# Optimization experiments

Measured on AMD Instinct MI355X. Metric: run time of the kernel, lower is better.

The kernel has to match this reference:

```python
import jax, jax.numpy as jnp
import numpy as np

# --- configuration matching setup_inputs ---
N_EVENTS = 4          # number of events in the ragged batch (row_splits has 5 entries)
HITS_PER_EVENT = 50000
K_CLUSTERS = 256      # max truth shower index per event
Q_MIN = 1.0
REPULSION_CONTRIB = 0.5
SCALE = 1.0
EPS = 1e-6


def setup_inputs() -> dict:
    key = jax.random.key(0)
    k1, k2 = jax.random.split(key)
    n = N_EVENTS * HITS_PER_EVENT
    coords = jax.random.normal(k1, (n, 3), dtype=jnp.float32)
    truth_indices = jax.random.randint(k2, (n, 1), 0, K_CLUSTERS, dtype=jnp.int32)
    row_splits = (jnp.arange(N_EVENTS + 1, dtype=jnp.int32) * HITS_PER_EVENT)
    return {"coords": coords, "truth_indices": truth_indices, "row_splits": row_splits}


def _oc_cluster_loss(coords, truth_indices):
    """Object-condensation attractive/repulsive potentials.

    coords:        [n, C] float clustering coordinates (n = E * Nev, equal splits)
    truth_indices: [n, 1] int cluster id per hit, in [0, K)
    Returns (V_att, V_rep) scalars, averaged over events.
    """
    C = coords.shape[1]
    x = coords.reshape(N_EVENTS, HITS_PER_EVENT, C)            # [E, N, C]
    t = truth_indices.reshape(N_EVENTS, HITS_PER_EVENT)        # [E, N]

    # beta_like = 0.5 (3-input path of LLClusterCoordinates) -> constant charge
    beta = jnp.float32(0.5)
    q_val = jnp.arctanh(beta) ** 2 + jnp.float32(Q_MIN)        # scalar
    q = jnp.full((N_EVENTS, HITS_PER_EVENT), q_val, dtype=coords.dtype)  # [E, N]

    # membership mask (one-hot over truth clusters)
    M = jax.nn.one_hot(t, K_CLUSTERS, dtype=coords.dtype)      # [E, N, K]
    qM = M * q[..., None]                                      # [E, N, K]

    # q-weighted average condensation point per cluster (use_average_cc_pos=True)
    sum_q = jnp.sum(qM, axis=1)                                # [E, K]
    x_cc = jnp.einsum('enk,enc->ekc', qM, x) / (sum_q[..., None] + EPS)  # [E, K, C]

    # charge of the condensation (max-beta) vertex per cluster
    q_alpha = jnp.max(qM, axis=1)                              # [E, K] (0 for empty clusters)

    # pairwise hit <-> condensation-point distances
    diff = x[:, :, None, :] - x_cc[:, None, :, :]              # [E, N, K, C]
    d2 = jnp.sum(diff * diff, axis=-1)                         # [E, N, K]
    d = jnp.sqrt(d2 + EPS)

    w = q[..., None] * q_alpha[:, None, :]                     # [E, N, K]
    n_per_ev = jnp.float32(HITS_PER_EVENT)

    V_att_ev = jnp.sum(M * w * d2, axis=(1, 2)) / n_per_ev                   # [E]
    V_rep_ev = jnp.sum((1.0 - M) * w * jax.nn.relu(1.0 - d), axis=(1, 2)) / n_per_ev
    return jnp.mean(V_att_ev), jnp.mean(V_rep_ev)


def reference(coords, truth_indices, row_splits):
    V_att, V_rep = _oc_cluster_loss(coords, truth_indices)
    lossval = SCALE * ((1.0 - REPULSION_CONTRIB) * V_att + REPULSION_CONTRIB * V_rep)
    # layer returns (inputs[0], lossval) when return_lossval=True
    return coords, lossval
```

## Files before the change

### kernel.cpp

```cpp
#include <hip/hip_runtime.h>

typedef unsigned long long ull;

#define E_EVENTS 4
#define NPE 50000
#define K_CL 256
#define QV 1.30173724f
#define QV2 (QV * QV)
#define EPSF 1e-6f
#define SB 64
#define BPE 196
#define LOSS_SCALE 2.5e-6f
#define LOSS_IDX (3 * E_EVENTS * NPE)

__global__ __launch_bounds__(256) void k_sums(const float* __restrict__ coords,
                                              const int* __restrict__ truth,
                                              float* __restrict__ partial,
                                              int* __restrict__ maxn) {
    __shared__ float s[4 * K_CL];
    int tid = threadIdx.x;
    #pragma unroll
    for (int i = 0; i < 4; ++i) s[tid + 256 * i] = 0.0f;
    __syncthreads();

    int e = blockIdx.x >> 6, blk = blockIdx.x & (SB - 1);
    if (blk == 0 && tid == 0) maxn[e] = 0;
    for (int local = blk * 256 + tid; local < NPE; local += SB * 256) {
        int h = e * NPE + local;
        int t = truth[h];
        atomicAdd(&s[t],            coords[3 * h]);
        atomicAdd(&s[K_CL + t],     coords[3 * h + 1]);
        atomicAdd(&s[2 * K_CL + t], coords[3 * h + 2]);
        atomicAdd(&s[3 * K_CL + t], 1.0f);
    }
    __syncthreads();

    float* g = partial + blockIdx.x * 1024;
    #pragma unroll
    for (int i = 0; i < 4; ++i) g[tid + 256 * i] = s[tid + 256 * i];
}

__global__ __launch_bounds__(1024) void k_cc(const float* __restrict__ partial,
                                             float4* __restrict__ cc,
                                             int* __restrict__ maxn,
                                             float* __restrict__ out) {
    __shared__ float4 red[16][64];
    int tid = threadIdx.x;
    int kl = tid & 63, chunk = tid >> 6;
    int e = blockIdx.x >> 2, kg = blockIdx.x & 3;
    int k = kg * 64 + kl;

    const float* base = partial + (e * SB + chunk * 4) * 1024 + k;
    float sx = 0.f, sy = 0.f, sz = 0.f, cn = 0.f;
    #pragma unroll
    for (int j = 0; j < 4; ++j) {
        const float* p = base + j * 1024;
        sx += p[0]; sy += p[256]; sz += p[512]; cn += p[768];
    }
    red[chunk][kl] = make_float4(sx, sy, sz, cn);
    __syncthreads();
    #pragma unroll
    for (int s = 8; s > 0; s >>= 1) {
        if (chunk < s) {
            float4 a = red[chunk][kl], o = red[chunk + s][kl];
            red[chunk][kl] = make_float4(a.x + o.x, a.y + o.y,
                                         a.z + o.z, a.w + o.w);
        }
        __syncthreads();
    }

    if (chunk == 0) {
        float4 t = red[0][kl];
        float inv = QV / (QV * t.w + EPSF);
        float cx = t.x * inv, cy = t.y * inv, cz = t.z * inv;
        float ccn = fmaf(cx, cx, fmaf(cy, cy, cz * cz));
        bool empty = (t.w == 0.0f);
        cc[e * K_CL + k] = empty ? make_float4(0.f, 0.f, 0.f, 1e9f)
                                 : make_float4(cx, cy, cz, ccn);
        float nrm = empty ? 0.f : __builtin_amdgcn_sqrtf(ccn);
        #pragma unroll
        for (int o = 32; o > 0; o >>= 1)
            nrm = fmaxf(nrm, __shfl_down(nrm, o, 64));
        if (kl == 0) atomicMax(&maxn[e], __float_as_int(nrm));
        if (blockIdx.x == 0 && tid == 0) out[LOSS_IDX] = 0.0f;
    }
}

__global__ __launch_bounds__(256) void k_fused(const float* __restrict__ coords,
                                               const int* __restrict__ truth,
                                               const float4* __restrict__ cc,
                                               const int* __restrict__ maxn,
                                               float* __restrict__ out) {
    __shared__ float4 hl[256];
    __shared__ float4 scc[K_CL];
    __shared__ int bcnt;
    __shared__ float wsum[4];
    int tid = threadIdx.x;
    int lane = tid & 63, wv = tid >> 6;
    int e = blockIdx.x / BPE;
    int local = (blockIdx.x - e * BPE) * 256 + tid;
    bool valid = local < NPE;

    scc[tid] = cc[e * K_CL + tid];
    if (tid == 0) bcnt = 0;
    float M = __int_as_float(maxn[e]);
    float th = 1.0f + M + 1e-3f;
    float th2 = th * th;
    __syncthreads();

    float att = 0.0f, pp = 1e30f, x = 0.f, y = 0.f, z = 0.f;
    if (valid) {
        int h = e * NPE + local;
        x = coords[3 * h]; y = coords[3 * h + 1]; z = coords[3 * h + 2];
        int t = truth[h];
        out[3 * h] = x; out[3 * h + 1] = y; out[3 * h + 2] = z;
        float4 c = scc[t];
        float dx = x - c.x, dy = y - c.y, dz = z - c.z;
        float d2o = fmaf(dx, dx, fmaf(dy, dy, dz * dz));
        float dno = __builtin_amdgcn_sqrtf(d2o + EPSF);
        att = QV2 * (d2o - fmaxf(0.0f, 1.0f - dno));
        pp = fmaf(x, x, fmaf(y, y, z * z));
    }

    bool inner = valid && (pp < th2);
    ull mask = __ballot(inner);
    int cnt = __popcll(mask);
    if (cnt > 0) {
        int leader = __ffsll(mask) - 1;
        int base = 0;
        if (lane == leader) base = atomicAdd(&bcnt, cnt);
        base = __shfl(base, leader, 64);
        if (inner) {
            int prefix = __popcll(mask & ((1ull << lane) - 1ull));
            hl[base + prefix] = make_float4(-2.0f * x, -2.0f * y, -2.0f * z,
                                            pp + EPSF);
        }
    }
    __syncthreads();

    float4 c0 = scc[lane], c1 = scc[lane + 64];
    float4 c2 = scc[lane + 128], c3 = scc[lane + 192];
    int n = bcnt;
    float rep = 0.0f;
    #pragma unroll 2
    for (int j = wv; j < n; j += 4) {
        float4 p = hl[j];
        float a0 = fmaf(p.x, c0.x, fmaf(p.y, c0.y, fmaf(p.z, c0.z, c0.w))) + p.w;
        float a1 = fmaf(p.x, c1.x, fmaf(p.y, c1.y, fmaf(p.z, c1.z, c1.w))) + p.w;
        float a2 = fmaf(p.x, c2.x, fmaf(p.y, c2.y, fmaf(p.z, c2.z, c2.w))) + p.w;
        float a3 = fmaf(p.x, c3.x, fmaf(p.y, c3.y, fmaf(p.z, c3.z, c3.w))) + p.w;
        rep += fmaxf(0.0f, 1.0f - __builtin_amdgcn_sqrtf(a0))
             + fmaxf(0.0f, 1.0f - __builtin_amdgcn_sqrtf(a1))
             + fmaxf(0.0f, 1.0f - __builtin_amdgcn_sqrtf(a2))
             + fmaxf(0.0f, 1.0f - __builtin_amdgcn_sqrtf(a3));
    }
    float contrib = att + QV2 * rep;

    #pragma unroll
    for (int o = 32; o > 0; o >>= 1) contrib += __shfl_down(contrib, o, 64);
    if (lane == 0) wsum[wv] = contrib;
    __syncthreads();
    if (tid == 0)
        atomicAdd(out + LOSS_IDX,
                  (wsum[0] + wsum[1] + wsum[2] + wsum[3]) * LOSS_SCALE);
}

extern "C" void kernel_launch(void* const* d_in, const int* in_sizes, int n_in,
                              void* d_out, int out_size, void* d_ws, size_t ws_size,
                              hipStream_t stream) {
    const float* coords = (const float*)d_in[0];
    const int*   truth  = (const int*)d_in[1];

    char* ws = (char*)d_ws;
    float*  partial = (float*)ws;
    float4* cc      = (float4*)(ws + (1 << 20));
    int*    maxn    = (int*)(ws + (1 << 20) + 16384);
    float*  out     = (float*)d_out;

    k_sums <<<E_EVENTS * SB, 256, 0, stream>>>(coords, truth, partial, maxn);
    k_cc   <<<16, 1024, 0, stream>>>(partial, cc, maxn, out);
    k_fused<<<E_EVENTS * BPE, 256, 0, stream>>>(coords, truth, cc, maxn, out);
}
```

Before: 83.21 us.

## Fuse sum, centroid and loss kernels into one cooperative kernel with grid syncs

Merges the three launches (per-cluster sums, centroid reduction, fused loss) into a single cooperative kernel separated by two grid-wide syncs. Coordinates and truth labels are loaded once and kept in registers across phases, so the second global read disappears. Each block now builds its own shared-memory histogram, which enlarges the partials buffer; the centroid step reduces these across 64 blocks. The cost is the grid barriers plus the requirement that all 784 blocks be co-resident.

```diff
diff --git a/kernel.cpp b/kernel.cpp
--- a/kernel.cpp
+++ b/kernel.cpp
@@ -1,4 +1,7 @@
 #include <hip/hip_runtime.h>
+#include <hip/hip_cooperative_groups.h>
+
+namespace cg = cooperative_groups;
 
 typedef unsigned long long ull;
 
@@ -8,99 +11,105 @@
 #define QV 1.30173724f
 #define QV2 (QV * QV)
 #define EPSF 1e-6f
-#define SB 64
 #define BPE 196
+#define NBLK (E_EVENTS * BPE)
+#define CCBLK 64
 #define LOSS_SCALE 2.5e-6f
 #define LOSS_IDX (3 * E_EVENTS * NPE)
 
-__global__ __launch_bounds__(256) void k_sums(const float* __restrict__ coords,
-                                              const int* __restrict__ truth,
-                                              float* __restrict__ partial,
-                                              int* __restrict__ maxn) {
-    __shared__ float s[4 * K_CL];
+__global__ __launch_bounds__(256, 4) void k_all(const float* __restrict__ coords,
+                                                const int* __restrict__ truth,
+                                                float* __restrict__ partial,
+                                                float4* __restrict__ cc,
+                                                int* __restrict__ maxn,
+                                                float* __restrict__ out) {
+    __shared__ float4 shA[256];
+    __shared__ float4 shB[256];
+    __shared__ int bcnt;
+    __shared__ float wsum[4];
+
+    cg::grid_group grid = cg::this_grid();
     int tid = threadIdx.x;
+    int lane = tid & 63, wv = tid >> 6;
+    int b = blockIdx.x;
+    int e = b / BPE, lb = b - e * BPE;
+    int local = lb * 256 + tid;
+    bool valid = local < NPE;
+
+    float* hist = (float*)shA;
     #pragma unroll
-    for (int i = 0; i < 4; ++i) s[tid + 256 * i] = 0.0f;
-    __syncthreads();
-
-    int e = blockIdx.x >> 6, blk = blockIdx.x & (SB - 1);
-    if (blk == 0 && tid == 0) maxn[e] = 0;
-    for (int local = blk * 256 + tid; local < NPE; local += SB * 256) {
-        int h = e * NPE + local;
-        int t = truth[h];
-        atomicAdd(&s[t],            coords[3 * h]);
-        atomicAdd(&s[K_CL + t],     coords[3 * h + 1]);
-        atomicAdd(&s[2 * K_CL + t], coords[3 * h + 2]);
-        atomicAdd(&s[3 * K_CL + t], 1.0f);
+    for (int i = 0; i < 4; ++i) hist[tid + 256 * i] = 0.0f;
+    if (tid == 0) {
+        if (lb == 0) maxn[e] = 0;
+        if (b == 0) out[LOSS_IDX] = 0.0f;
     }
     __syncthreads();
 
-    float* g = partial + blockIdx.x * 1024;
-    #pragma unroll
-    for (int i = 0; i < 4; ++i) g[tid + 256 * i] = s[tid + 256 * i];
-}
-
-__global__ __launch_bounds__(1024) void k_cc(const float* __restrict__ partial,
-                                             float4* __restrict__ cc,
-                                             int* __restrict__ maxn,
-                                             float* __restrict__ out) {
-    __shared__ float4 red[16][64];
-    int tid = threadIdx.x;
-    int kl = tid & 63, chunk = tid >> 6;
-    int e = blockIdx.x >> 2, kg = blockIdx.x & 3;
-    int k = kg * 64 + kl;
-
-    const float* base = partial + (e * SB + chunk * 4) * 1024 + k;
-    float sx = 0.f, sy = 0.f, sz = 0.f, cn = 0.f;
-    #pragma unroll
-    for (int j = 0; j < 4; ++j) {
-        const float* p = base + j * 1024;
-        sx += p[0]; sy += p[256]; sz += p[512]; cn += p[768];
+    float x = 0.f, y = 0.f, z = 0.f, pp = 1e30f;
+    int t = 0;
+    if (valid) {
+        int h = e * NPE + local;
+        x = coords[3 * h]; y = coords[3 * h + 1]; z = coords[3 * h + 2];
+        t = truth[h];
+        out[3 * h] = x; out[3 * h + 1] = y; out[3 * h + 2] = z;
+        pp = fmaf(x, x, fmaf(y, y, z * z));
+        atomicAdd(&hist[t],            x);
+        atomicAdd(&hist[K_CL + t],     y);
+        atomicAdd(&hist[2 * K_CL + t], z);
+        atomicAdd(&hist[3 * K_CL + t], 1.0f);
     }
-    red[chunk][kl] = make_float4(sx, sy, sz, cn);
     __syncthreads();
-    #pragma unroll
-    for (int s = 8; s > 0; s >>= 1) {
-        if (chunk < s) {
-            float4 a = red[chunk][kl], o = red[chunk + s][kl];
-            red[chunk][kl] = make_float4(a.x + o.x, a.y + o.y,
-                                         a.z + o.z, a.w + o.w);
-        }
-        __syncthreads();
+    {
+        float* g = partial + b * 1024;
+        #pragma unroll
+        for (int i = 0; i < 4; ++i) g[tid + 256 * i] = hist[tid + 256 * i];
     }
 
-    if (chunk == 0) {
-        float4 t = red[0][kl];
-        float inv = QV / (QV * t.w + EPSF);
-        float cx = t.x * inv, cy = t.y * inv, cz = t.z * inv;
-        float ccn = fmaf(cx, cx, fmaf(cy, cy, cz * cz));
-        bool empty = (t.w == 0.0f);
-        cc[e * K_CL + k] = empty ? make_float4(0.f, 0.f, 0.f, 1e9f)
-                                 : make_float4(cx, cy, cz, ccn);
-        float nrm = empty ? 0.f : __builtin_amdgcn_sqrtf(ccn);
+    grid.sync();
+
+    if (b < CCBLK) {
+        int e1 = b >> 4;
+        int kg = b & 15;
+        int kl = tid & 15, cgp = tid >> 4;
+        int k = kg * 16 + kl;
+        float sx = 0.f, sy = 0.f, sz = 0.f, cn = 0.f;
+        const float* base = partial + (e1 * BPE) * 1024 + k;
+        for (int c = cgp; c < BPE; c += 16) {
+            const float* p = base + c * 1024;
+            sx += p[0]; sy += p[256]; sz += p[512]; cn += p[768];
+        }
+        float4* red = shB;
+        red[cgp * 16 + kl] = make_float4(sx, sy, sz, cn);
+        __syncthreads();
         #pragma unroll
-        for (int o = 32; o > 0; o >>= 1)
-            nrm = fmaxf(nrm, __shfl_down(nrm, o, 64));
-        if (kl == 0) atomicMax(&maxn[e], __float_as_int(nrm));
-        if (blockIdx.x == 0 && tid == 0) out[LOSS_IDX] = 0.0f;
+        for (int s = 8; s > 0; s >>= 1) {
+            if (cgp < s) {
+                float4 a = red[cgp * 16 + kl], o = red[(cgp + s) * 16 + kl];
+                red[cgp * 16 + kl] = make_float4(a.x + o.x, a.y + o.y,
+                                                 a.z + o.z, a.w + o.w);
+            }
+            __syncthreads();
+        }
+        if (cgp == 0) {
+            float4 s4 = red[kl];
+            float inv = QV / (QV * s4.w + EPSF);
+            float cx = s4.x * inv, cy = s4.y * inv, cz = s4.z * inv;
+            float ccn = fmaf(cx, cx, fmaf(cy, cy, cz * cz));
+            bool empty = (s4.w == 0.0f);
+            cc[e1 * K_CL + k] = empty ? make_float4(0.f, 0.f, 0.f, 1e9f)
+                                      : make_float4(cx, cy, cz, ccn);
+            float nrm = empty ? 0.f : __builtin_amdgcn_sqrtf(ccn);
+            #pragma unroll
+            for (int o = 8; o > 0; o >>= 1)
+                nrm = fmaxf(nrm, __shfl_down(nrm, o, 16));
+            if (kl == 0) atomicMax(&maxn[e1], __float_as_int(nrm));
+        }
     }
-}
 
-__global__ __launch_bounds__(256) void k_fused(const float* __restrict__ coords,
-                                               const int* __restrict__ truth,
-                                               const float4* __restrict__ cc,
-                                               const int* __restrict__ maxn,
-                                               float* __restrict__ out) {
-    __shared__ float4 hl[256];
-    __shared__ float4 scc[K_CL];
-    __shared__ int bcnt;
-    __shared__ float wsum[4];
-    int tid = threadIdx.x;
-    int lane = tid & 63, wv = tid >> 6;
-    int e = blockIdx.x / BPE;
-    int local = (blockIdx.x - e * BPE) * 256 + tid;
-    bool valid = local < NPE;
+    grid.sync();
 
+    float4* scc = shA;
+    float4* hl  = shB;
     scc[tid] = cc[e * K_CL + tid];
     if (tid == 0) bcnt = 0;
     float M = __int_as_float(maxn[e]);
@@ -108,18 +117,13 @@
     float th2 = th * th;
     __syncthreads();
 
-    float att = 0.0f, pp = 1e30f, x = 0.f, y = 0.f, z = 0.f;
+    float att = 0.0f;
     if (valid) {
-        int h = e * NPE + local;
-        x = coords[3 * h]; y = coords[3 * h + 1]; z = coords[3 * h + 2];
-        int t = truth[h];
-        out[3 * h] = x; out[3 * h + 1] = y; out[3 * h + 2] = z;
         float4 c = scc[t];
         float dx = x - c.x, dy = y - c.y, dz = z - c.z;
         float d2o = fmaf(dx, dx, fmaf(dy, dy, dz * dz));
         float dno = __builtin_amdgcn_sqrtf(d2o + EPSF);
         att = QV2 * (d2o - fmaxf(0.0f, 1.0f - dno));
-        pp = fmaf(x, x, fmaf(y, y, z * z));
     }
 
     bool inner = valid && (pp < th2);
@@ -127,13 +131,13 @@
     int cnt = __popcll(mask);
     if (cnt > 0) {
         int leader = __ffsll(mask) - 1;
-        int base = 0;
-        if (lane == leader) base = atomicAdd(&bcnt, cnt);
-        base = __shfl(base, leader, 64);
+        int base0 = 0;
+        if (lane == leader) base0 = atomicAdd(&bcnt, cnt);
+        base0 = __shfl(base0, leader, 64);
         if (inner) {
             int prefix = __popcll(mask & ((1ull << lane) - 1ull));
-            hl[base + prefix] = make_float4(-2.0f * x, -2.0f * y, -2.0f * z,
-                                            pp + EPSF);
+            hl[base0 + prefix] = make_float4(-2.0f * x, -2.0f * y, -2.0f * z,
+                                             pp + EPSF);
         }
     }
     __syncthreads();
@@ -173,11 +177,12 @@
 
     char* ws = (char*)d_ws;
     float*  partial = (float*)ws;
-    float4* cc      = (float4*)(ws + (1 << 20));
-    int*    maxn    = (int*)(ws + (1 << 20) + 16384);
+    float4* cc      = (float4*)(ws + (4 << 20));
+    int*    maxn    = (int*)(ws + (4 << 20) + 16384);
     float*  out     = (float*)d_out;
 
-    k_sums <<<E_EVENTS * SB, 256, 0, stream>>>(coords, truth, partial, maxn);
-    k_cc   <<<16, 1024, 0, stream>>>(partial, cc, maxn, out);
-    k_fused<<<E_EVENTS * BPE, 256, 0, stream>>>(coords, truth, cc, maxn, out);
+    void* args[6] = {(void*)&coords, (void*)&truth, (void*)&partial,
+                     (void*)&cc, (void*)&maxn, (void*)&out};
+    hipLaunchCooperativeKernel((const void*)k_all, dim3(NBLK), dim3(256),
+                               args, 0, stream);
 }
```

Result: slower. 219.1 us (+163.4%).

## Fold centroid reduction into fused kernel and vectorize per-cluster sums

Applied to the files above, without the earlier changes.

Removes the separate centroid kernel. Each fused block now reduces the per-event partial sums itself, computes the condensation points and the max norm in shared memory, and so drops one launch and the global maxn atomics. The sums kernel uses float4/int4 vector loads with 1024-thread blocks and fewer blocks per event. The fused kernel moves to 512-thread blocks, which gives larger candidate lists. The cost is that every fused block redundantly reduces 16 partial records, and the sums kernel has less parallelism.

```diff
diff --git a/kernel.cpp b/kernel.cpp
--- a/kernel.cpp
+++ b/kernel.cpp
@@ -8,105 +8,89 @@
 #define QV 1.30173724f
 #define QV2 (QV * QV)
 #define EPSF 1e-6f
-#define SB 64
-#define BPE 196
+#define SB 16
+#define FB 512
+#define BPE 98
 #define LOSS_SCALE 2.5e-6f
 #define LOSS_IDX (3 * E_EVENTS * NPE)
 
-__global__ __launch_bounds__(256) void k_sums(const float* __restrict__ coords,
-                                              const int* __restrict__ truth,
-                                              float* __restrict__ partial,
-                                              int* __restrict__ maxn) {
+__global__ __launch_bounds__(1024) void k_sums(const float4* __restrict__ c4,
+                                               const int4* __restrict__ t4,
+                                               float4* __restrict__ partial,
+                                               float* __restrict__ out) {
     __shared__ float s[4 * K_CL];
     int tid = threadIdx.x;
-    #pragma unroll
-    for (int i = 0; i < 4; ++i) s[tid + 256 * i] = 0.0f;
+    s[tid] = 0.0f;
+    if (blockIdx.x == 0 && tid == 0) out[LOSS_IDX] = 0.0f;
     __syncthreads();
 
-    int e = blockIdx.x >> 6, blk = blockIdx.x & (SB - 1);
-    if (blk == 0 && tid == 0) maxn[e] = 0;
-    for (int local = blk * 256 + tid; local < NPE; local += SB * 256) {
-        int h = e * NPE + local;
-        int t = truth[h];
-        atomicAdd(&s[t],            coords[3 * h]);
-        atomicAdd(&s[K_CL + t],     coords[3 * h + 1]);
-        atomicAdd(&s[2 * K_CL + t], coords[3 * h + 2]);
-        atomicAdd(&s[3 * K_CL + t], 1.0f);
+    int e = blockIdx.x >> 4, blk = blockIdx.x & (SB - 1);
+    const float4* cb = c4 + e * (NPE * 3 / 4);
+    const int4*   tb = t4 + e * (NPE / 4);
+    for (int g = blk * 1024 + tid; g < NPE / 4; g += SB * 1024) {
+        float4 a = cb[3 * g], b = cb[3 * g + 1], c = cb[3 * g + 2];
+        int4 t = tb[g];
+        atomicAdd(&s[t.x], a.x); atomicAdd(&s[K_CL + t.x], a.y);
+        atomicAdd(&s[2 * K_CL + t.x], a.z); atomicAdd(&s[3 * K_CL + t.x], 1.0f);
+        atomicAdd(&s[t.y], a.w); atomicAdd(&s[K_CL + t.y], b.x);
+        atomicAdd(&s[2 * K_CL + t.y], b.y); atomicAdd(&s[3 * K_CL + t.y], 1.0f);
+        atomicAdd(&s[t.z], b.z); atomicAdd(&s[K_CL + t.z], b.w);
+        atomicAdd(&s[2 * K_CL + t.z], c.x); atomicAdd(&s[3 * K_CL + t.z], 1.0f);
+        atomicAdd(&s[t.w], c.y); atomicAdd(&s[K_CL + t.w], c.z);
+        atomicAdd(&s[2 * K_CL + t.w], c.w); atomicAdd(&s[3 * K_CL + t.w], 1.0f);
     }
     __syncthreads();
-
-    float* g = partial + blockIdx.x * 1024;
-    #pragma unroll
-    for (int i = 0; i < 4; ++i) g[tid + 256 * i] = s[tid + 256 * i];
+    if (tid < K_CL)
+        partial[blockIdx.x * K_CL + tid] =
+            make_float4(s[tid], s[K_CL + tid], s[2 * K_CL + tid], s[3 * K_CL + tid]);
 }
 
-__global__ __launch_bounds__(1024) void k_cc(const float* __restrict__ partial,
-                                             float4* __restrict__ cc,
-                                             int* __restrict__ maxn,
-                                             float* __restrict__ out) {
-    __shared__ float4 red[16][64];
+__global__ __launch_bounds__(512) void k_fused(const float* __restrict__ coords,
+                                               const int* __restrict__ truth,
+                                               const float4* __restrict__ partial,
+                                               float* __restrict__ out) {
+    __shared__ float4 scc[K_CL];
+    __shared__ float4 hl[FB];
+    __shared__ int bcnt;
+    __shared__ float wsum[8], wmax[4];
     int tid = threadIdx.x;
-    int kl = tid & 63, chunk = tid >> 6;
-    int e = blockIdx.x >> 2, kg = blockIdx.x & 3;
-    int k = kg * 64 + kl;
+    int lane = tid & 63, wv = tid >> 6;
+    int e = blockIdx.x / BPE;
+    int local = (blockIdx.x - e * BPE) * FB + tid;
+    bool valid = local < NPE;
+    if (tid == 0) bcnt = 0;
 
-    const float* base = partial + (e * SB + chunk * 4) * 1024 + k;
-    float sx = 0.f, sy = 0.f, sz = 0.f, cn = 0.f;
-    #pragma unroll
-    for (int j = 0; j < 4; ++j) {
-        const float* p = base + j * 1024;
-        sx += p[0]; sy += p[256]; sz += p[512]; cn += p[768];
+    {
+        int k = tid & 255, half = tid >> 8;
+        const float4* base = partial + e * SB * K_CL + half * 8 * K_CL + k;
+        float4 acc = make_float4(0.f, 0.f, 0.f, 0.f);
+        #pragma unroll
+        for (int c = 0; c < 8; ++c) {
+            float4 p = base[c * K_CL];
+            acc.x += p.x; acc.y += p.y; acc.z += p.z; acc.w += p.w;
+        }
+        hl[tid] = acc;
     }
-    red[chunk][kl] = make_float4(sx, sy, sz, cn);
     __syncthreads();
-    #pragma unroll
-    for (int s = 8; s > 0; s >>= 1) {
-        if (chunk < s) {
-            float4 a = red[chunk][kl], o = red[chunk + s][kl];
-            red[chunk][kl] = make_float4(a.x + o.x, a.y + o.y,
-                                         a.z + o.z, a.w + o.w);
-        }
-        __syncthreads();
-    }
-
-    if (chunk == 0) {
-        float4 t = red[0][kl];
-        float inv = QV / (QV * t.w + EPSF);
-        float cx = t.x * inv, cy = t.y * inv, cz = t.z * inv;
+    if (tid < K_CL) {
+        float4 a = hl[tid], b = hl[tid + 256];
+        float sx = a.x + b.x, sy = a.y + b.y, sz = a.z + b.z, cn = a.w + b.w;
+        float inv = QV / (QV * cn + EPSF);
+        float cx = sx * inv, cy = sy * inv, cz = sz * inv;
         float ccn = fmaf(cx, cx, fmaf(cy, cy, cz * cz));
-        bool empty = (t.w == 0.0f);
-        cc[e * K_CL + k] = empty ? make_float4(0.f, 0.f, 0.f, 1e9f)
-                                 : make_float4(cx, cy, cz, ccn);
+        bool empty = (cn == 0.0f);
+        scc[tid] = empty ? make_float4(0.f, 0.f, 0.f, 1e9f)
+                         : make_float4(cx, cy, cz, ccn);
         float nrm = empty ? 0.f : __builtin_amdgcn_sqrtf(ccn);
         #pragma unroll
         for (int o = 32; o > 0; o >>= 1)
             nrm = fmaxf(nrm, __shfl_down(nrm, o, 64));
-        if (kl == 0) atomicMax(&maxn[e], __float_as_int(nrm));
-        if (blockIdx.x == 0 && tid == 0) out[LOSS_IDX] = 0.0f;
+        if (lane == 0) wmax[wv] = nrm;
     }
-}
-
-__global__ __launch_bounds__(256) void k_fused(const float* __restrict__ coords,
-                                               const int* __restrict__ truth,
-                                               const float4* __restrict__ cc,
-                                               const int* __restrict__ maxn,
-                                               float* __restrict__ out) {
-    __shared__ float4 hl[256];
-    __shared__ float4 scc[K_CL];
-    __shared__ int bcnt;
-    __shared__ float wsum[4];
-    int tid = threadIdx.x;
-    int lane = tid & 63, wv = tid >> 6;
-    int e = blockIdx.x / BPE;
-    int local = (blockIdx.x - e * BPE) * 256 + tid;
-    bool valid = local < NPE;
-
-    scc[tid] = cc[e * K_CL + tid];
-    if (tid == 0) bcnt = 0;
-    float M = __int_as_float(maxn[e]);
+    __syncthreads();
+    float M = fmaxf(fmaxf(wmax[0], wmax[1]), fmaxf(wmax[2], wmax[3]));
     float th = 1.0f + M + 1e-3f;
     float th2 = th * th;
-    __syncthreads();
 
     float att = 0.0f, pp = 1e30f, x = 0.f, y = 0.f, z = 0.f;
     if (valid) {
@@ -127,13 +111,13 @@
     int cnt = __popcll(mask);
     if (cnt > 0) {
         int leader = __ffsll(mask) - 1;
-        int base = 0;
-        if (lane == leader) base = atomicAdd(&bcnt, cnt);
-        base = __shfl(base, leader, 64);
+        int b0 = 0;
+        if (lane == leader) b0 = atomicAdd(&bcnt, cnt);
+        b0 = __shfl(b0, leader, 64);
         if (inner) {
             int prefix = __popcll(mask & ((1ull << lane) - 1ull));
-            hl[base + prefix] = make_float4(-2.0f * x, -2.0f * y, -2.0f * z,
-                                            pp + EPSF);
+            hl[b0 + prefix] = make_float4(-2.0f * x, -2.0f * y, -2.0f * z,
+                                          pp + EPSF);
         }
     }
     __syncthreads();
@@ -143,7 +127,7 @@
     int n = bcnt;
     float rep = 0.0f;
     #pragma unroll 2
-    for (int j = wv; j < n; j += 4) {
+    for (int j = wv; j < n; j += 8) {
         float4 p = hl[j];
         float a0 = fmaf(p.x, c0.x, fmaf(p.y, c0.y, fmaf(p.z, c0.z, c0.w))) + p.w;
         float a1 = fmaf(p.x, c1.x, fmaf(p.y, c1.y, fmaf(p.z, c1.z, c1.w))) + p.w;
@@ -160,9 +144,11 @@
     for (int o = 32; o > 0; o >>= 1) contrib += __shfl_down(contrib, o, 64);
     if (lane == 0) wsum[wv] = contrib;
     __syncthreads();
-    if (tid == 0)
-        atomicAdd(out + LOSS_IDX,
-                  (wsum[0] + wsum[1] + wsum[2] + wsum[3]) * LOSS_SCALE);
+    if (tid == 0) {
+        float ssum = wsum[0] + wsum[1] + wsum[2] + wsum[3]
+                   + wsum[4] + wsum[5] + wsum[6] + wsum[7];
+        atomicAdd(out + LOSS_IDX, ssum * LOSS_SCALE);
+    }
 }
 
 extern "C" void kernel_launch(void* const* d_in, const int* in_sizes, int n_in,
@@ -171,13 +157,10 @@
     const float* coords = (const float*)d_in[0];
     const int*   truth  = (const int*)d_in[1];
 
-    char* ws = (char*)d_ws;
-    float*  partial = (float*)ws;
-    float4* cc      = (float4*)(ws + (1 << 20));
-    int*    maxn    = (int*)(ws + (1 << 20) + 16384);
+    float4* partial = (float4*)d_ws;
     float*  out     = (float*)d_out;
 
-    k_sums <<<E_EVENTS * SB, 256, 0, stream>>>(coords, truth, partial, maxn);
-    k_cc   <<<16, 1024, 0, stream>>>(partial, cc, maxn, out);
-    k_fused<<<E_EVENTS * BPE, 256, 0, stream>>>(coords, truth, cc, maxn, out);
+    k_sums <<<E_EVENTS * SB, 1024, 0, stream>>>((const float4*)coords,
+                                                (const int4*)truth, partial, out);
+    k_fused<<<E_EVENTS * BPE, FB, 0, stream>>>(coords, truth, partial, out);
 }
```

Result: slower. 90.86 us (+9.2%).
